# Optimization experiments

Measured on AMD Instinct MI355X. Metric: run time of the kernel, lower is better.

The kernel has to match this reference:

```python
import jax, jax.numpy as jnp
import numpy as np

D, H, DFF = 1024, 16, 4096
HD = D // H
NEG = -1e9  # finite stand-in for -inf causal mask (grad-safe)


def layer_norm(x, g, b, eps=1e-5):
    mu = jnp.mean(x, axis=-1, keepdims=True)
    var = jnp.mean(jnp.square(x - mu), axis=-1, keepdims=True)
    return (x - mu) * jax.lax.rsqrt(var + eps) * g + b


def setup_inputs() -> dict:
    key = jax.random.key(0)
    ks = jax.random.split(key, 16)
    B, T = 2, 2048
    x = jax.random.normal(ks[0], (B, T, D), jnp.float32)
    causal_mask = jnp.where(jnp.triu(jnp.ones((T, T), bool), k=1), NEG, 0.0).astype(jnp.float32)
    ema_attn = jax.random.uniform(ks[1], (H, T, T), jnp.float32)
    # normalize EMA rows like attention weights would be
    ema_attn = ema_attn / jnp.sum(ema_attn, axis=-1, keepdims=True)
    s = 0.02
    p = {
        'x': x, 'causal_mask': causal_mask, 'ema_attn': ema_attn,
        'log_tau_attn': jnp.array(0.0, jnp.float32),
        'Wq': jax.random.normal(ks[2], (D, D), jnp.float32) * s,
        'bq': jnp.zeros((D,), jnp.float32),
        'Wk': jax.random.normal(ks[3], (D, D), jnp.float32) * s,
        'bk': jnp.zeros((D,), jnp.float32),
        'Wv': jax.random.normal(ks[4], (D, D), jnp.float32) * s,
        'bv': jnp.zeros((D,), jnp.float32),
        'Wo': jax.random.normal(ks[5], (D, D), jnp.float32) * s,
        'bo': jnp.zeros((D,), jnp.float32),
        'W1': jax.random.normal(ks[6], (DFF, D), jnp.float32) * s,
        'b1': jnp.zeros((DFF,), jnp.float32),
        'W2': jax.random.normal(ks[7], (D, DFF), jnp.float32) * s,
        'b2': jnp.zeros((D,), jnp.float32),
        'g1': jnp.ones((D,), jnp.float32), 'beta1': jnp.zeros((D,), jnp.float32),
        'g2': jnp.ones((D,), jnp.float32), 'beta2': jnp.zeros((D,), jnp.float32),
    }
    return p


def reference(x, causal_mask, ema_attn, log_tau_attn, Wq, bq, Wk, bk, Wv, bv,
              Wo, bo, W1, b1, W2, b2, g1, beta1, g2, beta2):
    B, T, _ = x.shape
    # habituation bias: -tau_a * mean over heads of the EMA attention
    tau_a = jnp.exp(log_tau_attn)
    habit_bias = -(tau_a * ema_attn).mean(0)            # (T, T)
    attn_mask = causal_mask + habit_bias                # (T, T)

    # multi-head self-attention (torch MHA math, dropout=0 / eval)
    q = (x @ Wq.T + bq).reshape(B, T, H, HD)
    k = (x @ Wk.T + bk).reshape(B, T, H, HD)
    v = (x @ Wv.T + bv).reshape(B, T, H, HD)
    scores = jnp.einsum('bthd,bshd->bhts', q, k) / jnp.sqrt(jnp.float32(HD))
    scores = scores + attn_mask[None, None]             # (B, H, T, T)
    attn = jax.nn.softmax(scores, axis=-1)
    ctx = jnp.einsum('bhts,bshd->bthd', attn, v).reshape(B, T, D)
    attn_out = ctx @ Wo.T + bo

    # residual + norm, then FFN (GELU), residual + norm
    h = layer_norm(x + attn_out, g1, beta1)
    ff = (jax.nn.gelu(h @ W1.T + b1) @ W2.T) + b2
    out = layer_norm(h + ff, g2, beta2)
    return out
```

## Files before the change

kernel.cpp:

```cpp
#include <hip/hip_runtime.h>
#include <hip/hip_bf16.h>
#include <math.h>

#define T_SEQ 2048
#define D_MODEL 1024
#define BT 4096

typedef __bf16 bf16;
typedef __bf16 bf16x8 __attribute__((ext_vector_type(8)));
typedef __bf16 bf16x4 __attribute__((ext_vector_type(4)));
typedef float f32x4 __attribute__((ext_vector_type(4)));

__device__ __forceinline__ void gload_lds16(const bf16* g, bf16* l) {
  __builtin_amdgcn_global_load_lds(
      (__attribute__((address_space(1))) void*)(g),
      (__attribute__((address_space(3))) void*)(l), 16, 0, 0);
}

__global__ __launch_bounds__(256) void k_mask(const float* __restrict__ causal,
                                              const float* __restrict__ ema,
                                              const float* __restrict__ logtau,
                                              bf16* __restrict__ mask) {
  const size_t i = (size_t)blockIdx.x * 256 + threadIdx.x;
  const float c = -__expf(logtau[0]) * (1.0f / 16.0f);
  float4 v = ((const float4*)causal)[i];
  float a0 = v.x, a1 = v.y, a2 = v.z, a3 = v.w;
#pragma unroll
  for (int h = 0; h < 16; ++h) {
    float4 e = ((const float4*)(ema + (size_t)h * T_SEQ * T_SEQ))[i];
    a0 += c * e.x; a1 += c * e.y; a2 += c * e.z; a3 += c * e.w;
  }
  bf16x4 o;
  o[0] = (bf16)a0; o[1] = (bf16)a1; o[2] = (bf16)a2; o[3] = (bf16)a3;
  ((bf16x4*)mask)[i] = o;
}

struct CvtArgs {
  const float* src[7];
  bf16* dst[7];
  int cum[8];
};
__global__ __launch_bounds__(256) void k_cvt_all(CvtArgs a) {
  const int i = blockIdx.x * 256 + threadIdx.x;
  if (i >= a.cum[7]) return;
  int s = 0;
#pragma unroll
  for (int k = 1; k < 7; ++k) s += (i >= a.cum[k]);
  const int j = i - a.cum[s];
  float4 v = ((const float4*)a.src[s])[j];
  bf16x4 o;
  o[0] = (bf16)v.x; o[1] = (bf16)v.y; o[2] = (bf16)v.z; o[3] = (bf16)v.w;
  ((bf16x4*)a.dst[s])[j] = o;
}

__global__ void k_bias3(const float* __restrict__ bq, const float* __restrict__ bk,
                        const float* __restrict__ bv, float* __restrict__ o) {
  const int i = blockIdx.x * 256 + threadIdx.x;
  o[i] = (i < 1024) ? bq[i] : (i < 2048 ? bk[i - 1024] : bv[i - 2048]);
}

__device__ __forceinline__ float gelu_tanh(float x) {
  return 0.5f * x * (1.0f + tanhf(0.7978845608028654f * (x + 0.044715f * x * x * x)));
}

template <int EPI>
__global__ __launch_bounds__(512, 2) void k_gemm_ring(const bf16* __restrict__ A,
                                                      const bf16* __restrict__ B,
                                                      const float* __restrict__ bias,
                                                      const float* __restrict__ resid,
                                                      float* __restrict__ outf,
                                                      bf16* __restrict__ outb,
                                                      int K, int N) {
  __shared__ bf16 sA[3][256 * 64];
  __shared__ bf16 sB[3][128 * 64];
  const int tid = threadIdx.x;
  const int m0 = blockIdx.x * 256, n0 = blockIdx.y * 128;
  const int lane = tid & 63;
  const int w = tid >> 6, wr = w >> 1, wc = w & 1;
  const int lr = lane & 15, lg = lane >> 4;

  const int srow = lane >> 3;
  const int schunk = (lane & 7) ^ srow;

  auto stage = [&](int buf, int kt) {
    const int k0 = kt << 6;
#pragma unroll
    for (int e = 0; e < 4; ++e) {
      const int r = w * 32 + e * 8 + srow;
      gload_lds16(A + (size_t)(m0 + r) * K + k0 + schunk * 8,
                  &sA[buf][(w * 32 + e * 8) * 64 + lane * 8]);
    }
#pragma unroll
    for (int e = 0; e < 2; ++e) {
      const int r = w * 16 + e * 8 + srow;
      gload_lds16(B + (size_t)(n0 + r) * K + k0 + schunk * 8,
                  &sB[buf][(w * 16 + e * 8) * 64 + lane * 8]);
    }
  };

  f32x4 acc[4][4] = {};

  stage(0, 0);
  stage(1, 1);
  stage(2, 2);

  const int KT = K >> 6;
  for (int t = 0; t < KT; ++t) {
    if (t <= KT - 3)      asm volatile("s_waitcnt vmcnt(12)" ::: "memory");
    else if (t == KT - 2) asm volatile("s_waitcnt vmcnt(6)" ::: "memory");
    else                  asm volatile("s_waitcnt vmcnt(0)" ::: "memory");
    __builtin_amdgcn_s_barrier();

    const int buf = t % 3;
    const char* pA = (const char*)sA[buf];
    const char* pB = (const char*)sB[buf];
    bf16x8 af[4][2], bfr[4][2];
#pragma unroll
    for (int m = 0; m < 4; ++m) {
      const int row = wr * 64 + m * 16 + lr;
#pragma unroll
      for (int kk = 0; kk < 2; ++kk) {
        const unsigned off =
            (unsigned)(row * 128) + (((unsigned)((kk << 2) | lg)) ^ (unsigned)(row & 7)) * 16u;
        af[m][kk] = *(const bf16x8*)(pA + off);
      }
    }
#pragma unroll
    for (int n = 0; n < 4; ++n) {
      const int row = wc * 64 + n * 16 + lr;
#pragma unroll
      for (int kk = 0; kk < 2; ++kk) {
        const unsigned off =
            (unsigned)(row * 128) + (((unsigned)((kk << 2) | lg)) ^ (unsigned)(row & 7)) * 16u;
        bfr[n][kk] = *(const bf16x8*)(pB + off);
      }
    }
    asm volatile("s_waitcnt lgkmcnt(0)" ::: "memory");
    __builtin_amdgcn_s_barrier();
    if (t < KT - 3) stage(buf, t + 3);

    __builtin_amdgcn_s_setprio(1);
#pragma unroll
    for (int m = 0; m < 4; ++m)
#pragma unroll
      for (int n = 0; n < 4; ++n)
#pragma unroll
        for (int kk = 0; kk < 2; ++kk)
          acc[m][n] = __builtin_amdgcn_mfma_f32_16x16x32_bf16(af[m][kk], bfr[n][kk],
                                                              acc[m][n], 0, 0, 0);
    __builtin_amdgcn_s_setprio(0);
  }

  const int row0 = m0 + wr * 64 + (lane >> 4) * 4;
  const int col0 = n0 + wc * 64 + lr;
#pragma unroll
  for (int m = 0; m < 4; ++m) {
#pragma unroll
    for (int n = 0; n < 4; ++n) {
      const int col = col0 + n * 16;
      const float bv = bias[col];
#pragma unroll
      for (int r = 0; r < 4; ++r) {
        const int row = row0 + m * 16 + r;
        float v = acc[m][n][r] + bv;
        if (EPI == 0) {
          outb[(size_t)row * N + col] = (bf16)v;
        } else if (EPI == 1) {
          v += resid[(size_t)row * N + col];
          outf[(size_t)row * N + col] = v;
        } else {
          outb[(size_t)row * N + col] = (bf16)gelu_tanh(v);
        }
      }
    }
  }
}

template <int EPI>
__global__ __launch_bounds__(256, 2) void k_gemm_ring2(const bf16* __restrict__ A,
                                                       const bf16* __restrict__ B,
                                                       const float* __restrict__ bias,
                                                       const float* __restrict__ resid,
                                                       float* __restrict__ outf,
                                                       bf16* __restrict__ outb,
                                                       int K, int N) {
  __shared__ bf16 sA[2][128 * 64];
  __shared__ bf16 sB[2][128 * 64];
  const int tid = threadIdx.x;
  const int m0 = blockIdx.x * 128, n0 = blockIdx.y * 128;
  const int lane = tid & 63;
  const int w = tid >> 6, wr = w >> 1, wc = w & 1;
  const int lr = lane & 15, lg = lane >> 4;

  const int srow = lane >> 3;
  const int schunk = (lane & 7) ^ srow;

  auto stage = [&](int buf, int kt) {
    const int k0 = kt << 6;
#pragma unroll
    for (int e = 0; e < 4; ++e) {
      const int r = w * 32 + e * 8 + srow;
      gload_lds16(A + (size_t)(m0 + r) * K + k0 + schunk * 8,
                  &sA[buf][(w * 32 + e * 8) * 64 + lane * 8]);
      gload_lds16(B + (size_t)(n0 + r) * K + k0 + schunk * 8,
                  &sB[buf][(w * 32 + e * 8) * 64 + lane * 8]);
    }
  };

  f32x4 acc[4][4] = {};

  stage(0, 0);
  stage(1, 1);

  const int KT = K >> 6;
  for (int t = 0; t < KT; ++t) {
    if (t < KT - 1) asm volatile("s_waitcnt vmcnt(8)" ::: "memory");
    else            asm volatile("s_waitcnt vmcnt(0)" ::: "memory");
    __builtin_amdgcn_s_barrier();

    const int buf = t & 1;
    const char* pA = (const char*)sA[buf];
    const char* pB = (const char*)sB[buf];
    bf16x8 af[4][2], bfr[4][2];
#pragma unroll
    for (int m = 0; m < 4; ++m) {
      const int row = wr * 64 + m * 16 + lr;
#pragma unroll
      for (int kk = 0; kk < 2; ++kk) {
        const unsigned off =
            (unsigned)(row * 128) + (((unsigned)((kk << 2) | lg)) ^ (unsigned)(row & 7)) * 16u;
        af[m][kk] = *(const bf16x8*)(pA + off);
      }
    }
#pragma unroll
    for (int n = 0; n < 4; ++n) {
      const int row = wc * 64 + n * 16 + lr;
#pragma unroll
      for (int kk = 0; kk < 2; ++kk) {
        const unsigned off =
            (unsigned)(row * 128) + (((unsigned)((kk << 2) | lg)) ^ (unsigned)(row & 7)) * 16u;
        bfr[n][kk] = *(const bf16x8*)(pB + off);
      }
    }
    asm volatile("s_waitcnt lgkmcnt(0)" ::: "memory");
    __builtin_amdgcn_s_barrier();
    if (t + 2 < KT) stage(buf, t + 2);

    __builtin_amdgcn_s_setprio(1);
#pragma unroll
    for (int m = 0; m < 4; ++m)
#pragma unroll
      for (int n = 0; n < 4; ++n)
#pragma unroll
        for (int kk = 0; kk < 2; ++kk)
          acc[m][n] = __builtin_amdgcn_mfma_f32_16x16x32_bf16(af[m][kk], bfr[n][kk],
                                                              acc[m][n], 0, 0, 0);
    __builtin_amdgcn_s_setprio(0);
  }

  const int row0 = m0 + wr * 64 + (lane >> 4) * 4;
  const int col0 = n0 + wc * 64 + lr;
#pragma unroll
  for (int m = 0; m < 4; ++m) {
#pragma unroll
    for (int n = 0; n < 4; ++n) {
      const int col = col0 + n * 16;
      const float bv = bias[col];
#pragma unroll
      for (int r = 0; r < 4; ++r) {
        const int row = row0 + m * 16 + r;
        float v = acc[m][n][r] + bv;
        if (EPI == 0) {
          outb[(size_t)row * N + col] = (bf16)v;
        } else if (EPI == 1) {
          v += resid[(size_t)row * N + col];
          outf[(size_t)row * N + col] = v;
        } else {
          outb[(size_t)row * N + col] = (bf16)gelu_tanh(v);
        }
      }
    }
  }
}

__global__ __launch_bounds__(256) void k_attn(const bf16* __restrict__ qkv,
                                              const bf16* __restrict__ maskb,
                                              bf16* __restrict__ ctx) {
  const int bh = blockIdx.x;
  const int qt = blockIdx.y;
  const int b = bh >> 4, h = bh & 15;
  const int tid = threadIdx.x, w = tid >> 6, lane = tid & 63;
  const int lr = lane & 15, lg = lane >> 4;

  __shared__ bf16 sK[2][64 * 64];
  __shared__ bf16 sVt[2][64 * 72];
  __shared__ bf16 sM[2][64 * 64];
  __shared__ bf16 sP[4][16 * 64];

  const size_t rs = 3072;
  const bf16* base = qkv + (size_t)b * T_SEQ * rs + h * 64;
  const int q0b = qt * 64;
  const int qrow = w * 16 + lr;

  bf16x8 qf[2];
#pragma unroll
  for (int kk = 0; kk < 2; ++kk) {
    bf16x8 q = *(const bf16x8*)(base + (size_t)(q0b + qrow) * rs + kk * 32 + lg * 8);
#pragma unroll
    for (int j = 0; j < 8; ++j) qf[kk][j] = (bf16)((float)q[j] * 0.125f);
  }

  const int srow = lane >> 3;
  const int scol = lane & 7;

  auto issueKM = [&](int s0, bf16* sKb, bf16* sMb) {
#pragma unroll
    for (int e = 0; e < 2; ++e) {
      const int kb = w * 16 + e * 8;
      const int r = kb + srow;
      const int cs = 8 * (scol ^ (r & 7));
      gload_lds16(base + (size_t)(s0 + r) * rs + 1024 + cs, &sKb[kb * 64 + lane * 8]);
      gload_lds16(maskb + (size_t)(q0b + r) * T_SEQ + s0 + cs, &sMb[kb * 64 + lane * 8]);
    }
  };
  auto loadV = [&](int s0, bf16x8 vv[2]) {
#pragma unroll
    for (int t = 0; t < 2; ++t) {
      const int c = w * 64 + lane + t * 256;
      vv[t] = *(const bf16x8*)(base + (size_t)(s0 + (c >> 3)) * rs + 2048 + (c & 7) * 8);
    }
  };
  auto writeV = [&](const bf16x8 vv[2], bf16* sVtb) {
    char* pb = (char*)sVtb;
#pragma unroll
    for (int t = 0; t < 2; ++t) {
      const int c = w * 64 + lane + t * 256;
      const int s = c >> 3, dc = c & 7;
#pragma unroll
      for (int j = 0; j < 8; ++j) {
        const unsigned ba = ((unsigned)((dc * 8 + j) * 72 + s) * 2) ^ ((unsigned)dc << 4);
        *(bf16*)(pb + ba) = vv[t][j];
      }
    }
  };

  float m_r = -3.0e38f, l_r = 0.0f;
  f32x4 o[4] = {};

  const float L2E = 1.44269504088896f;
  const int nt = qt + 1;
  const unsigned swzq = (unsigned)(lr & 7) << 4;

  {
    bf16x8 v0[2];
    loadV(0, v0);
    issueKM(0, sK[0], sM[0]);
    writeV(v0, sVt[0]);
  }
  __syncthreads();

  int cur = 0;
  for (int t = 0; t < nt; ++t, cur ^= 1) {
    const bool pf = (t + 1 < nt);
    bf16x8 vv[2];
    if (pf) {
      loadV((t + 1) * 64, vv);
      issueKM((t + 1) * 64, sK[cur ^ 1], sM[cur ^ 1]);
    }

    const char* sMc = (const char*)sM[cur];
    f32x4 sc[4];
#pragma unroll
    for (int n = 0; n < 4; ++n) {
      const unsigned ba = ((unsigned)(qrow * 128 + n * 32 + lg * 8)) ^ swzq;
      bf16x4 mk = *(const bf16x4*)(sMc + ba);
#pragma unroll
      for (int j = 0; j < 4; ++j) sc[n][j] = (float)mk[j];
    }

    const char* sKc = (const char*)sK[cur];
    __builtin_amdgcn_s_setprio(1);
#pragma unroll
    for (int n = 0; n < 4; ++n) {
      const int key = n * 16 + lr;
#pragma unroll
      for (int kk = 0; kk < 2; ++kk) {
        const unsigned boff =
            (unsigned)(key * 128 + kk * 64 + lg * 16) ^ ((unsigned)(key & 7) << 4);
        bf16x8 kf = *(const bf16x8*)(sKc + boff);
        sc[n] = __builtin_amdgcn_mfma_f32_16x16x32_bf16(kf, qf[kk], sc[n], 0, 0, 0);
      }
    }
    __builtin_amdgcn_s_setprio(0);

    float mx = -3.0e38f;
#pragma unroll
    for (int n = 0; n < 4; ++n)
#pragma unroll
      for (int j = 0; j < 4; ++j) mx = fmaxf(mx, sc[n][j]);
    mx = fmaxf(mx, __shfl_xor(mx, 16));
    mx = fmaxf(mx, __shfl_xor(mx, 32));

    if (!__all(mx <= m_r + 8.0f)) {
      const float mnew = fmaxf(m_r, mx);
      const float alpha = exp2f((m_r - mnew) * L2E);
      m_r = mnew;
      l_r *= alpha;
      float a4[4];
#pragma unroll
      for (int j = 0; j < 4; ++j) a4[j] = __shfl(alpha, (lane & 48) | (lg * 4 + j));
#pragma unroll
      for (int dt = 0; dt < 4; ++dt)
#pragma unroll
        for (int j = 0; j < 4; ++j) o[dt][j] *= a4[j];
    }

    const float mL2 = m_r * L2E;
    float ps = 0.0f;
    float pn[4][4];
#pragma unroll
    for (int n = 0; n < 4; ++n)
#pragma unroll
      for (int j = 0; j < 4; ++j) {
        const float p = exp2f(sc[n][j] * L2E - mL2);
        pn[n][j] = p;
        ps += p;
      }
    ps += __shfl_xor(ps, 16);
    ps += __shfl_xor(ps, 32);
    l_r += ps;

    if (pf) writeV(vv, sVt[cur ^ 1]);

    char* sPw = (char*)sP[w];
#pragma unroll
    for (int n = 0; n < 4; ++n) {
      bf16x4 pb;
#pragma unroll
      for (int j = 0; j < 4; ++j) pb[j] = (bf16)pn[n][j];
      *(bf16x4*)(sPw + (((unsigned)(lr * 128 + n * 32 + lg * 8)) ^ swzq)) = pb;
    }

    bf16x8 pa[2];
#pragma unroll
    for (int kk = 0; kk < 2; ++kk)
      pa[kk] = *(const bf16x8*)(sPw + (((unsigned)(lr * 128 + kk * 64 + lg * 16)) ^ swzq));
    const char* sVc = (const char*)sVt[cur];
    __builtin_amdgcn_s_setprio(1);
#pragma unroll
    for (int dt = 0; dt < 4; ++dt) {
      const int dd = dt * 16 + lr;
#pragma unroll
      for (int kk = 0; kk < 2; ++kk) {
        const unsigned ba =
            ((unsigned)(dd * 72 + kk * 32 + lg * 8) * 2) ^ ((unsigned)((dd >> 3) & 7) << 4);
        bf16x8 vb = *(const bf16x8*)(sVc + ba);
        o[dt] = __builtin_amdgcn_mfma_f32_16x16x32_bf16(pa[kk], vb, o[dt], 0, 0, 0);
      }
    }
    __builtin_amdgcn_s_setprio(0);
    __syncthreads();
  }

  float linv[4];
#pragma unroll
  for (int j = 0; j < 4; ++j) linv[j] = 1.0f / __shfl(l_r, (lane & 48) | (lg * 4 + j));
#pragma unroll
  for (int j = 0; j < 4; ++j) {
    const size_t row = (size_t)b * T_SEQ + q0b + w * 16 + lg * 4 + j;
#pragma unroll
    for (int dt = 0; dt < 4; ++dt)
      ctx[row * D_MODEL + h * 64 + dt * 16 + lr] = (bf16)(o[dt][j] * linv[j]);
  }
}

__global__ __launch_bounds__(256) void k_ln(const float* __restrict__ in,
                                            const float* __restrict__ g,
                                            const float* __restrict__ be,
                                            float* __restrict__ out,
                                            bf16* __restrict__ outb) {
  const int row = blockIdx.x, tid = threadIdx.x;
  const float4 v = *(const float4*)(in + (size_t)row * 1024 + tid * 4);
  float s = v.x + v.y + v.z + v.w;
  float s2 = v.x * v.x + v.y * v.y + v.z * v.z + v.w * v.w;
#pragma unroll
  for (int d = 1; d < 64; d <<= 1) { s += __shfl_xor(s, d); s2 += __shfl_xor(s2, d); }
  __shared__ float red[8];
  const int w = tid >> 6;
  if ((tid & 63) == 0) { red[w] = s; red[4 + w] = s2; }
  __syncthreads();
  s = red[0] + red[1] + red[2] + red[3];
  s2 = red[4] + red[5] + red[6] + red[7];
  const float mu = s * (1.0f / 1024.0f);
  const float var = s2 * (1.0f / 1024.0f) - mu * mu;
  const float inv = rsqrtf(var + 1e-5f);
  const int col = tid * 4;
  const float4 gv = *(const float4*)(g + col);
  const float4 bv = *(const float4*)(be + col);
  float4 y;
  y.x = (v.x - mu) * inv * gv.x + bv.x;
  y.y = (v.y - mu) * inv * gv.y + bv.y;
  y.z = (v.z - mu) * inv * gv.z + bv.z;
  y.w = (v.w - mu) * inv * gv.w + bv.w;
  *(float4*)(out + (size_t)row * 1024 + col) = y;
  if (outb) {
    bf16x4 ob;
    ob[0] = (bf16)y.x; ob[1] = (bf16)y.y; ob[2] = (bf16)y.z; ob[3] = (bf16)y.w;
    *(bf16x4*)(outb + (size_t)row * 1024 + col) = ob;
  }
}

extern "C" void kernel_launch(void* const* d_in, const int* in_sizes, int n_in,
                              void* d_out, int out_size, void* d_ws, size_t ws_size,
                              hipStream_t stream) {
  const float* x      = (const float*)d_in[0];
  const float* causal = (const float*)d_in[1];
  const float* ema    = (const float*)d_in[2];
  const float* logtau = (const float*)d_in[3];
  const float* Wq = (const float*)d_in[4];
  const float* bq = (const float*)d_in[5];
  const float* Wk = (const float*)d_in[6];
  const float* bk = (const float*)d_in[7];
  const float* Wv = (const float*)d_in[8];
  const float* bv = (const float*)d_in[9];
  const float* Wo = (const float*)d_in[10];
  const float* bo = (const float*)d_in[11];
  const float* W1 = (const float*)d_in[12];
  const float* b1 = (const float*)d_in[13];
  const float* W2 = (const float*)d_in[14];
  const float* b2 = (const float*)d_in[15];
  const float* g1  = (const float*)d_in[16];
  const float* be1 = (const float*)d_in[17];
  const float* g2  = (const float*)d_in[18];
  const float* be2 = (const float*)d_in[19];
  float* out = (float*)d_out;

  char* ws = (char*)d_ws;
  bf16*  maskb = (bf16*)(ws + 0);
  bf16*  x_bf  = (bf16*)(ws + (16UL << 20));
  bf16*  wqkv  = (bf16*)(ws + (24UL << 20));
  bf16*  wo_bf = (bf16*)(ws + (30UL << 20));
  bf16*  w1_bf = (bf16*)(ws + (32UL << 20));
  bf16*  w2_bf = (bf16*)(ws + (40UL << 20));
  float* bqkv  = (float*)(ws + (48UL << 20));
  bf16*  qkv   = (bf16*)(ws + (49UL << 20));
  bf16*  ctxb  = (bf16*)(ws + (73UL << 20));
  float* h_pre = (float*)(ws + (81UL << 20));
  float* hbuf  = (float*)(ws + (97UL << 20));
  bf16*  h_bf  = (bf16*)(ws + (113UL << 20));
  bf16*  ff1   = (bf16*)(ws + (121UL << 20));
  float* out_pre = (float*)(ws + 0);

  const dim3 blk(256);
  const dim3 blk512(512);

  k_mask<<<dim3(4096), blk, 0, stream>>>(causal, ema, logtau, maskb);

  CvtArgs ca;
  ca.src[0] = x;  ca.dst[0] = x_bf;
  ca.src[1] = Wq; ca.dst[1] = wqkv;
  ca.src[2] = Wk; ca.dst[2] = wqkv + (1UL << 20);
  ca.src[3] = Wv; ca.dst[3] = wqkv + (2UL << 20);
  ca.src[4] = Wo; ca.dst[4] = wo_bf;
  ca.src[5] = W1; ca.dst[5] = w1_bf;
  ca.src[6] = W2; ca.dst[6] = w2_bf;
  ca.cum[0] = 0;
  ca.cum[1] = 1048576;
  ca.cum[2] = 1048576 + 262144;
  ca.cum[3] = 1048576 + 524288;
  ca.cum[4] = 1048576 + 786432;
  ca.cum[5] = 2097152;
  ca.cum[6] = 2097152 + 1048576;
  ca.cum[7] = 4194304;
  k_cvt_all<<<dim3(16384), blk, 0, stream>>>(ca);
  k_bias3<<<dim3(12), blk, 0, stream>>>(bq, bk, bv, bqkv);

  k_gemm_ring<0><<<dim3(16, 24), blk512, 0, stream>>>(x_bf, wqkv, bqkv, nullptr, nullptr,
                                                      qkv, 1024, 3072);

  k_attn<<<dim3(32, 32), blk, 0, stream>>>(qkv, maskb, ctxb);

  k_gemm_ring2<1><<<dim3(32, 8), blk, 0, stream>>>(ctxb, wo_bf, bo, x, h_pre, nullptr,
                                                   1024, 1024);

  k_ln<<<dim3(4096), blk, 0, stream>>>(h_pre, g1, be1, hbuf, h_bf);

  k_gemm_ring<2><<<dim3(16, 32), blk512, 0, stream>>>(h_bf, w1_bf, b1, nullptr, nullptr,
                                                      ff1, 1024, 4096);

  k_gemm_ring2<1><<<dim3(32, 8), blk, 0, stream>>>(ff1, w2_bf, b2, hbuf, out_pre, nullptr,
                                                   4096, 1024);

  k_ln<<<dim3(4096), blk, 0, stream>>>(out_pre, g2, be2, out, nullptr);
}
```

Baseline: 363.5 us.

## Use 256x256 double-buffered GEMM tiles and skip masked mask tiles

The QKV and FFN1 GEMMs move from a 256x128 triple-buffered tile to a 256x256 double-buffered tile. Each wave now covers 128x64, and the two k-halves of each stage are split so LDS reads of the second half overlap the MFMAs of the first. The mask kernel becomes a 2D tile grid that returns early for tiles above the causal diagonal, cutting EMA reads roughly in half. This relies on attention never reading the unwritten upper mask tiles. The bigger GEMM tiles halve the block count, which risks fewer resident blocks and less tail balance, and they raise register pressure.

```diff
diff --git a/kernel.cpp b/kernel.cpp
--- a/kernel.cpp
+++ b/kernel.cpp
@@ -21,18 +21,27 @@
                                               const float* __restrict__ ema,
                                               const float* __restrict__ logtau,
                                               bf16* __restrict__ mask) {
-  const size_t i = (size_t)blockIdx.x * 256 + threadIdx.x;
+  const int qt = blockIdx.x, st = blockIdx.y;
+  if (st > qt) return;
+  const int t = threadIdx.x;
   const float c = -__expf(logtau[0]) * (1.0f / 16.0f);
-  float4 v = ((const float4*)causal)[i];
-  float a0 = v.x, a1 = v.y, a2 = v.z, a3 = v.w;
-#pragma unroll
-  for (int h = 0; h < 16; ++h) {
-    float4 e = ((const float4*)(ema + (size_t)h * T_SEQ * T_SEQ))[i];
-    a0 += c * e.x; a1 += c * e.y; a2 += c * e.z; a3 += c * e.w;
-  }
-  bf16x4 o;
-  o[0] = (bf16)a0; o[1] = (bf16)a1; o[2] = (bf16)a2; o[3] = (bf16)a3;
-  ((bf16x4*)mask)[i] = o;
+  const int r0 = t >> 4;
+  const int cc = t & 15;
+#pragma unroll
+  for (int rr = 0; rr < 4; ++rr) {
+    const size_t q = (size_t)qt * 64 + r0 + rr * 16;
+    const size_t f4 = q * 512 + st * 16 + cc;
+    float4 v = ((const float4*)causal)[f4];
+    float a0 = v.x, a1 = v.y, a2 = v.z, a3 = v.w;
+#pragma unroll
+    for (int h = 0; h < 16; ++h) {
+      float4 e = ((const float4*)(ema + (size_t)h * T_SEQ * T_SEQ))[f4];
+      a0 += c * e.x; a1 += c * e.y; a2 += c * e.z; a3 += c * e.w;
+    }
+    bf16x4 o;
+    o[0] = (bf16)a0; o[1] = (bf16)a1; o[2] = (bf16)a2; o[3] = (bf16)a3;
+    ((bf16x4*)mask)[f4] = o;
+  }
 }
 
 struct CvtArgs {
@@ -64,19 +73,19 @@
 }
 
 template <int EPI>
-__global__ __launch_bounds__(512, 2) void k_gemm_ring(const bf16* __restrict__ A,
-                                                      const bf16* __restrict__ B,
-                                                      const float* __restrict__ bias,
-                                                      const float* __restrict__ resid,
-                                                      float* __restrict__ outf,
-                                                      bf16* __restrict__ outb,
-                                                      int K, int N) {
-  __shared__ bf16 sA[3][256 * 64];
-  __shared__ bf16 sB[3][128 * 64];
+__global__ __launch_bounds__(512, 2) void k_gemm_big(const bf16* __restrict__ A,
+                                                     const bf16* __restrict__ B,
+                                                     const float* __restrict__ bias,
+                                                     const float* __restrict__ resid,
+                                                     float* __restrict__ outf,
+                                                     bf16* __restrict__ outb,
+                                                     int K, int N) {
+  __shared__ bf16 sA[2][256 * 64];
+  __shared__ bf16 sB[2][256 * 64];
   const int tid = threadIdx.x;
-  const int m0 = blockIdx.x * 256, n0 = blockIdx.y * 128;
+  const int m0 = blockIdx.x * 256, n0 = blockIdx.y * 256;
   const int lane = tid & 63;
-  const int w = tid >> 6, wr = w >> 1, wc = w & 1;
+  const int w = tid >> 6, wr = w >> 2, wc = w & 3;
   const int lr = lane & 15, lg = lane >> 4;
 
   const int srow = lane >> 3;
@@ -89,72 +98,77 @@
       const int r = w * 32 + e * 8 + srow;
       gload_lds16(A + (size_t)(m0 + r) * K + k0 + schunk * 8,
                   &sA[buf][(w * 32 + e * 8) * 64 + lane * 8]);
-    }
-#pragma unroll
-    for (int e = 0; e < 2; ++e) {
-      const int r = w * 16 + e * 8 + srow;
       gload_lds16(B + (size_t)(n0 + r) * K + k0 + schunk * 8,
-                  &sB[buf][(w * 16 + e * 8) * 64 + lane * 8]);
+                  &sB[buf][(w * 32 + e * 8) * 64 + lane * 8]);
     }
   };
 
-  f32x4 acc[4][4] = {};
+  f32x4 acc[8][4] = {};
 
   stage(0, 0);
   stage(1, 1);
-  stage(2, 2);
 
   const int KT = K >> 6;
   for (int t = 0; t < KT; ++t) {
-    if (t <= KT - 3)      asm volatile("s_waitcnt vmcnt(12)" ::: "memory");
-    else if (t == KT - 2) asm volatile("s_waitcnt vmcnt(6)" ::: "memory");
-    else                  asm volatile("s_waitcnt vmcnt(0)" ::: "memory");
+    if (t < KT - 1) asm volatile("s_waitcnt vmcnt(8)" ::: "memory");
+    else            asm volatile("s_waitcnt vmcnt(0)" ::: "memory");
     __builtin_amdgcn_s_barrier();
 
-    const int buf = t % 3;
+    const int buf = t & 1;
     const char* pA = (const char*)sA[buf];
     const char* pB = (const char*)sB[buf];
-    bf16x8 af[4][2], bfr[4][2];
-#pragma unroll
-    for (int m = 0; m < 4; ++m) {
-      const int row = wr * 64 + m * 16 + lr;
-#pragma unroll
-      for (int kk = 0; kk < 2; ++kk) {
-        const unsigned off =
-            (unsigned)(row * 128) + (((unsigned)((kk << 2) | lg)) ^ (unsigned)(row & 7)) * 16u;
-        af[m][kk] = *(const bf16x8*)(pA + off);
-      }
+
+    bf16x8 a0[8], b0[4];
+#pragma unroll
+    for (int m = 0; m < 8; ++m) {
+      const int row = wr * 128 + m * 16 + lr;
+      a0[m] = *(const bf16x8*)(pA + (unsigned)(row * 128) +
+                               (((unsigned)lg) ^ (unsigned)(row & 7)) * 16u);
     }
 #pragma unroll
     for (int n = 0; n < 4; ++n) {
       const int row = wc * 64 + n * 16 + lr;
-#pragma unroll
-      for (int kk = 0; kk < 2; ++kk) {
-        const unsigned off =
-            (unsigned)(row * 128) + (((unsigned)((kk << 2) | lg)) ^ (unsigned)(row & 7)) * 16u;
-        bfr[n][kk] = *(const bf16x8*)(pB + off);
-      }
+      b0[n] = *(const bf16x8*)(pB + (unsigned)(row * 128) +
+                               (((unsigned)lg) ^ (unsigned)(row & 7)) * 16u);
+    }
+    __builtin_amdgcn_s_setprio(1);
+#pragma unroll
+    for (int m = 0; m < 8; ++m)
+#pragma unroll
+      for (int n = 0; n < 4; ++n)
+        acc[m][n] = __builtin_amdgcn_mfma_f32_16x16x32_bf16(a0[m], b0[n], acc[m][n], 0, 0, 0);
+    __builtin_amdgcn_s_setprio(0);
+
+    bf16x8 a1[8], b1[4];
+#pragma unroll
+    for (int m = 0; m < 8; ++m) {
+      const int row = wr * 128 + m * 16 + lr;
+      a1[m] = *(const bf16x8*)(pA + (unsigned)(row * 128) +
+                               (((unsigned)(4 | lg)) ^ (unsigned)(row & 7)) * 16u);
+    }
+#pragma unroll
+    for (int n = 0; n < 4; ++n) {
+      const int row = wc * 64 + n * 16 + lr;
+      b1[n] = *(const bf16x8*)(pB + (unsigned)(row * 128) +
+                               (((unsigned)(4 | lg)) ^ (unsigned)(row & 7)) * 16u);
     }
     asm volatile("s_waitcnt lgkmcnt(0)" ::: "memory");
     __builtin_amdgcn_s_barrier();
-    if (t < KT - 3) stage(buf, t + 3);
+    if (t + 2 < KT) stage(buf, t + 2);
 
     __builtin_amdgcn_s_setprio(1);
 #pragma unroll
-    for (int m = 0; m < 4; ++m)
+    for (int m = 0; m < 8; ++m)
 #pragma unroll
       for (int n = 0; n < 4; ++n)
-#pragma unroll
-        for (int kk = 0; kk < 2; ++kk)
-          acc[m][n] = __builtin_amdgcn_mfma_f32_16x16x32_bf16(af[m][kk], bfr[n][kk],
-                                                              acc[m][n], 0, 0, 0);
+        acc[m][n] = __builtin_amdgcn_mfma_f32_16x16x32_bf16(a1[m], b1[n], acc[m][n], 0, 0, 0);
     __builtin_amdgcn_s_setprio(0);
   }
 
-  const int row0 = m0 + wr * 64 + (lane >> 4) * 4;
+  const int row0 = m0 + wr * 128 + (lane >> 4) * 4;
   const int col0 = n0 + wc * 64 + lr;
 #pragma unroll
-  for (int m = 0; m < 4; ++m) {
+  for (int m = 0; m < 8; ++m) {
 #pragma unroll
     for (int n = 0; n < 4; ++n) {
       const int col = col0 + n * 16;
@@ -554,7 +568,7 @@
   const dim3 blk(256);
   const dim3 blk512(512);
 
-  k_mask<<<dim3(4096), blk, 0, stream>>>(causal, ema, logtau, maskb);
+  k_mask<<<dim3(32, 32), blk, 0, stream>>>(causal, ema, logtau, maskb);
 
   CvtArgs ca;
   ca.src[0] = x;  ca.dst[0] = x_bf;
@@ -575,8 +589,8 @@
   k_cvt_all<<<dim3(16384), blk, 0, stream>>>(ca);
   k_bias3<<<dim3(12), blk, 0, stream>>>(bq, bk, bv, bqkv);
 
-  k_gemm_ring<0><<<dim3(16, 24), blk512, 0, stream>>>(x_bf, wqkv, bqkv, nullptr, nullptr,
-                                                      qkv, 1024, 3072);
+  k_gemm_big<0><<<dim3(16, 12), blk512, 0, stream>>>(x_bf, wqkv, bqkv, nullptr, nullptr,
+                                                     qkv, 1024, 3072);
 
   k_attn<<<dim3(32, 32), blk, 0, stream>>>(qkv, maskb, ctxb);
 
@@ -585,8 +599,8 @@
 
   k_ln<<<dim3(4096), blk, 0, stream>>>(h_pre, g1, be1, hbuf, h_bf);
 
-  k_gemm_ring<2><<<dim3(16, 32), blk512, 0, stream>>>(h_bf, w1_bf, b1, nullptr, nullptr,
-                                                      ff1, 1024, 4096);
+  k_gemm_big<2><<<dim3(16, 16), blk512, 0, stream>>>(h_bf, w1_bf, b1, nullptr, nullptr,
+                                                     ff1, 1024, 4096);
 
   k_gemm_ring2<1><<<dim3(32, 8), blk, 0, stream>>>(ff1, w2_bf, b2, hbuf, out_pre, nullptr,
                                                    4096, 1024);
```

After: 321.4 us. 1.13x faster.
